# Kernel tuning notes

Measured on AMD Instinct MI355X. Metric: run time of the kernel, lower is better.

## Reference

```python
import jax, jax.numpy as jnp
import numpy as np

B, T = 4, 2048          # batch, seq_len
D, H = 2048, 4096       # input_dim, router hidden_dim
E, O = 16, 2048         # num_experts, expert_output_dim
TAU = 0.5               # forward default tau


def setup_inputs() -> dict:
    key = jax.random.key(0)
    kx, k1, k2, k3, k4, k5, k6 = jax.random.split(key, 7)
    s = 0.02
    return {
        "x": jax.random.normal(kx, (B, T, D), dtype=jnp.float32),
        "W1": jax.random.normal(k1, (D, H), dtype=jnp.float32) * s,
        "b1": jnp.zeros((H,), dtype=jnp.float32),
        "W2": jax.random.normal(k2, (H, E), dtype=jnp.float32) * s,
        "b2": jnp.zeros((E,), dtype=jnp.float32),
        "We": jax.random.normal(k3, (E, D, O), dtype=jnp.float32) * s,
        "be": jnp.zeros((E, O), dtype=jnp.float32),
    }


def reference(x, W1, b1, W2, b2, We, be):
    # Router: Linear -> ReLU -> Linear -> softmax
    h = jax.nn.relu(jnp.einsum("btd,dh->bth", x, W1) + b1)
    logits = jnp.einsum("bth,he->bte", h, W2) + b2
    probs = jax.nn.softmax(logits, axis=-1)                 # [B,T,E]
    max_p = jnp.max(probs, axis=-1, keepdims=True)
    mask = probs >= TAU * max_p                              # [B,T,E] bool
    k_per_token = jnp.sum(mask, axis=-1)                     # [B,T] int
    gates = jnp.where(mask, probs, 0.0)                      # masked router probs
    # Per-expert dense Linear, masked weighted accumulate (E=16 is a fixed,
    # structurally distinct set; loop is over experts, not data dims).
    out = jnp.zeros((B, T, O), dtype=x.dtype)
    for i in range(E):
        expert_out = jnp.einsum("btd,do->bto", x, We[i]) + be[i]
        out = out + gates[..., i:i + 1] * expert_out
    return out, k_per_token
```

## Files before the change

### kernel.cpp

```cpp
#include <hip/hip_runtime.h>
#include <stdint.h>

#define M_TOK 8192
#define DDIM  2048
#define HDIM  4096
#define NEXP  16
#define ODIM  2048

typedef __attribute__((ext_vector_type(8))) __bf16 bf16x8;
typedef __attribute__((ext_vector_type(4))) float  f32x4;

__device__ __forceinline__ unsigned short f2bf(float f) {
    unsigned int u = __float_as_uint(f);
    unsigned int r = (u + 0x7FFFu + ((u >> 16) & 1u)) >> 16;
    return (unsigned short)r;
}
__device__ __forceinline__ float bf2f(unsigned short s) {
    return __uint_as_float(((unsigned int)s) << 16);
}

template <int CTRL>
__device__ __forceinline__ float dpp_mov(float x) {
    return __int_as_float(
        __builtin_amdgcn_update_dpp(0, __float_as_int(x), CTRL, 0xF, 0xF, true));
}
__device__ __forceinline__ float swz_xor4(float x) {
    return __int_as_float(__builtin_amdgcn_ds_swizzle(__float_as_int(x), 0x101F));
}


__global__ void split_x_kernel(const float* __restrict__ x,
                               ushort* __restrict__ xh, ushort* __restrict__ xl) {
    size_t i = ((size_t)blockIdx.x * 256 + threadIdx.x) * 4;
    float4 v = *(const float4*)(x + i);
    float f[4] = {v.x, v.y, v.z, v.w};
    ushort hu[4], lu[4];
#pragma unroll
    for (int u = 0; u < 4; ++u) {
        hu[u] = f2bf(f[u]);
        lu[u] = f2bf(f[u] - bf2f(hu[u]));
    }
    *(ushort4*)(xh + i) = make_ushort4(hu[0], hu[1], hu[2], hu[3]);
    *(ushort4*)(xl + i) = make_ushort4(lu[0], lu[1], lu[2], lu[3]);
}

__global__ void transpose_split_w1_kernel(const float* __restrict__ W1,
                                          ushort* __restrict__ th, ushort* __restrict__ tl) {
    __shared__ float tile[64][65];
    int h0 = (blockIdx.x & 63) * 64;
    int d0 = (blockIdx.x >> 6) * 64;
    int r = threadIdx.x >> 4;
    int c = (threadIdx.x & 15) * 4;
#pragma unroll
    for (int rr = 0; rr < 4; ++rr) {
        int row = rr * 16 + r;
        float4 v = *(const float4*)(W1 + (size_t)(d0 + row) * HDIM + h0 + c);
        tile[row][c + 0] = v.x; tile[row][c + 1] = v.y;
        tile[row][c + 2] = v.z; tile[row][c + 3] = v.w;
    }
    __syncthreads();
#pragma unroll
    for (int rr = 0; rr < 4; ++rr) {
        int hrow = rr * 16 + r;
        ushort hu[4], lu[4];
#pragma unroll
        for (int u = 0; u < 4; ++u) {
            float f = tile[c + u][hrow];
            hu[u] = f2bf(f);
            lu[u] = f2bf(f - bf2f(hu[u]));
        }
        size_t o = (size_t)(h0 + hrow) * DDIM + d0 + c;
        *(ushort4*)(th + o) = make_ushort4(hu[0], hu[1], hu[2], hu[3]);
        *(ushort4*)(tl + o) = make_ushort4(lu[0], lu[1], lu[2], lu[3]);
    }
}

__global__ void transpose_we_kernel(const float* __restrict__ We, ushort* __restrict__ wt) {
    __shared__ float tile[64][65];
    int e = blockIdx.y;
    int o0 = (blockIdx.x & 31) * 64;
    int d0 = (blockIdx.x >> 5) * 64;
    const float* src = We + (size_t)e * DDIM * ODIM;
    ushort* dst = wt + (size_t)e * ODIM * DDIM;
    int r = threadIdx.x >> 4;
    int c = (threadIdx.x & 15) * 4;
#pragma unroll
    for (int rr = 0; rr < 4; ++rr) {
        int row = rr * 16 + r;
        float4 v = *(const float4*)(src + (size_t)(d0 + row) * ODIM + o0 + c);
        tile[row][c + 0] = v.x; tile[row][c + 1] = v.y;
        tile[row][c + 2] = v.z; tile[row][c + 3] = v.w;
    }
    __syncthreads();
#pragma unroll
    for (int rr = 0; rr < 4; ++rr) {
        int orow = rr * 16 + r;
        ushort hu[4];
#pragma unroll
        for (int u = 0; u < 4; ++u) hu[u] = f2bf(tile[c + u][orow]);
        *(ushort4*)(dst + (size_t)(o0 + orow) * DDIM + d0 + c) =
            make_ushort4(hu[0], hu[1], hu[2], hu[3]);
    }
}


__device__ __forceinline__ void stage_tile(const ushort* __restrict__ g0, int ld,
                                           ushort* lds0, int wave, int lane) {
#pragma unroll
    for (int j = 0; j < 4; ++j) {
        int L = wave * 256 + j * 64 + lane;
        int m = L >> 3;
        int kc = (L & 7) ^ (m & 7);
        const ushort* gp = g0 + (size_t)m * ld + kc * 8;
        ushort* lp = lds0 + (size_t)(wave * 256 + j * 64) * 8;
        __builtin_amdgcn_global_load_lds(
            (const __attribute__((address_space(1))) void*)gp,
            (__attribute__((address_space(3))) void*)lp, 16, 0, 0);
    }
}

__device__ __forceinline__ bf16x8 ldfrag(const ushort* lds0, int row, int kc) {
    return *(const bf16x8*)(lds0 + ((row << 3) + (kc ^ (row & 7))) * 8);
}

__device__ __forceinline__ void mfma_step(const ushort* As, const ushort* Bs,
                                          int wm, int wn, int mrow, int q,
                                          f32x4 (&acc)[4][4]) {
#pragma unroll
    for (int s = 0; s < 2; ++s) {
        bf16x8 af[4], bfr[4];
#pragma unroll
        for (int i = 0; i < 4; ++i) af[i] = ldfrag(As, wm + i * 16 + mrow, s * 4 + q);
#pragma unroll
        for (int j = 0; j < 4; ++j) bfr[j] = ldfrag(Bs, wn + j * 16 + mrow, s * 4 + q);
#pragma unroll
        for (int i = 0; i < 4; ++i)
#pragma unroll
            for (int j = 0; j < 4; ++j)
                acc[i][j] = __builtin_amdgcn_mfma_f32_16x16x32_bf16(
                    af[i], bfr[j], acc[i][j], 0, 0, 0);
    }
}

__global__ __launch_bounds__(256, 2) void gemm1_kernel(
    const ushort* __restrict__ xh, const ushort* __restrict__ xl,
    const ushort* __restrict__ wh, const ushort* __restrict__ wl,
    const float* __restrict__ b1, const float* __restrict__ W2,
    float* __restrict__ logits) {
    __shared__ ushort As0[8192];
    __shared__ ushort Bs0[8192];
    __shared__ ushort As1[8192];
    __shared__ ushort Bs1[8192];
    const int tile_m = (blockIdx.x & 63) << 7;
    const int tile_n = (blockIdx.x >> 6) << 7;
    const int tid = threadIdx.x;
    const int wave = tid >> 6, lane = tid & 63;
    const int q = lane >> 4, mrow = lane & 15;
    const int wm = (wave >> 1) << 6, wn = (wave & 1) << 6;
    f32x4 acc[4][4];
#pragma unroll
    for (int i = 0; i < 4; ++i)
#pragma unroll
        for (int j = 0; j < 4; ++j) acc[i][j] = {0.f, 0.f, 0.f, 0.f};

#define SRC_A(t) ((((t) >> 5) == 1 ? xl : xh) + (size_t)tile_m * DDIM + (((t) & 31) << 6))
#define SRC_B(t) ((((t) >> 5) == 2 ? wl : wh) + (size_t)tile_n * DDIM + (((t) & 31) << 6))

    stage_tile(SRC_A(0), DDIM, As0, wave, lane);
    stage_tile(SRC_B(0), DDIM, Bs0, wave, lane);
    __syncthreads();

    for (int it = 0; it < 96; it += 2) {
        stage_tile(SRC_A(it + 1), DDIM, As1, wave, lane);
        stage_tile(SRC_B(it + 1), DDIM, Bs1, wave, lane);
        mfma_step(As0, Bs0, wm, wn, mrow, q, acc);
        __syncthreads();
        if (it + 2 < 96) {
            stage_tile(SRC_A(it + 2), DDIM, As0, wave, lane);
            stage_tile(SRC_B(it + 2), DDIM, Bs0, wave, lane);
        }
        mfma_step(As1, Bs1, wm, wn, mrow, q, acc);
        __syncthreads();
    }
#undef SRC_A
#undef SRC_B

    float b1v[4];
    f32x4 w2r[4][4];
#pragma unroll
    for (int j = 0; j < 4; ++j) {
        const int cc = tile_n + wn + j * 16 + mrow;
        b1v[j] = b1[cc];
        const float4* wp = (const float4*)(W2 + (size_t)cc * NEXP);
#pragma unroll
        for (int qq = 0; qq < 4; ++qq) {
            float4 v = wp[qq];
            w2r[j][qq] = (f32x4){v.x, v.y, v.z, v.w};
        }
    }
    float* part = (float*)As0;
    const int w01 = wave & 1;
    const bool pb0 = (mrow & 1) != 0, pb1 = (mrow & 2) != 0;
    const bool pb2 = (mrow & 4) != 0, pb3 = (mrow & 8) != 0;
    const int E = (mrow & 3) | ((mrow & 8) >> 1) | ((mrow & 4) << 1);
#pragma unroll
    for (int i = 0; i < 4; ++i) {
#pragma unroll
        for (int r = 0; r < 4; ++r) {
            const int rl = wm + i * 16 + q * 4 + r;
            float ll[16];
#pragma unroll
            for (int e = 0; e < 16; ++e) ll[e] = 0.f;
#pragma unroll
            for (int j = 0; j < 4; ++j) {
                float v = acc[i][j][r] + b1v[j];
                v = v > 0.f ? v : 0.f;
#pragma unroll
                for (int e = 0; e < 16; ++e)
                    ll[e] = fmaf(v, w2r[j][e >> 2][e & 3], ll[e]);
            }
            float s1[8];
#pragma unroll
            for (int e2 = 0; e2 < 8; ++e2) {
                float a = ll[2 * e2], b = ll[2 * e2 + 1];
                float y = pb0 ? b : a, z = pb0 ? a : b;
                s1[e2] = y + dpp_mov<0xB1>(z);
            }
            float s2[4];
#pragma unroll
            for (int e2 = 0; e2 < 4; ++e2) {
                float a = s1[2 * e2], b = s1[2 * e2 + 1];
                float y = pb1 ? b : a, z = pb1 ? a : b;
                s2[e2] = y + dpp_mov<0x4E>(z);
            }
            float s3[2];
#pragma unroll
            for (int e2 = 0; e2 < 2; ++e2) {
                float a = s2[2 * e2], b = s2[2 * e2 + 1];
                float y = pb3 ? b : a, z = pb3 ? a : b;
                s3[e2] = y + dpp_mov<0x128>(z);
            }
            {
                float a = s3[0], b = s3[1];
                float y = pb2 ? b : a, z = pb2 ? a : b;
                float fin = y + swz_xor4(z);
                part[(size_t)(w01 * 128 + rl) * 16 + E] = fin;
            }
        }
    }
    __syncthreads();
    for (int idx = tid; idx < 2048; idx += 256) {
        float s = part[idx] + part[2048 + idx];
        atomicAdd(&logits[(size_t)(tile_m + (idx >> 4)) * NEXP + (idx & 15)], s);
    }
}

__global__ void gates_kernel(const float* __restrict__ logits,
                             const float* __restrict__ b2,
                             float* __restrict__ gates, float* __restrict__ kout,
                             int* __restrict__ cnt, int* __restrict__ list) {
    const int t = blockIdx.x * 256 + threadIdx.x;
    float l[16];
    const float4* lp = (const float4*)(logits + (size_t)t * 16);
#pragma unroll
    for (int i = 0; i < 4; ++i) {
        float4 v = lp[i];
        l[i * 4] = v.x; l[i * 4 + 1] = v.y; l[i * 4 + 2] = v.z; l[i * 4 + 3] = v.w;
    }
#pragma unroll
    for (int i = 0; i < 16; ++i) l[i] += b2[i];
    float lmax = l[0];
#pragma unroll
    for (int i = 1; i < 16; ++i) lmax = fmaxf(lmax, l[i]);
    float p[16], S = 0.f;
#pragma unroll
    for (int i = 0; i < 16; ++i) { p[i] = expf(l[i] - lmax); S += p[i]; }
#pragma unroll
    for (int i = 0; i < 16; ++i) p[i] /= S;
    float pmax = p[0];
#pragma unroll
    for (int i = 1; i < 16; ++i) pmax = fmaxf(pmax, p[i]);
    const float thr = 0.5f * pmax;
    int k = 0;
    float g[16];
#pragma unroll
    for (int i = 0; i < 16; ++i) {
        bool m = p[i] >= thr;
        g[i] = m ? p[i] : 0.f;
        k += m ? 1 : 0;
        if (m) {
            int pos = atomicAdd(&cnt[i], 1);
            list[i * M_TOK + pos] = t;
        }
    }
    float4* gp = (float4*)(gates + (size_t)t * 16);
#pragma unroll
    for (int i = 0; i < 4; ++i)
        gp[i] = make_float4(g[i * 4], g[i * 4 + 1], g[i * 4 + 2], g[i * 4 + 3]);
    kout[t] = (float)k;
}

__global__ void init_out_kernel(const float* __restrict__ gates,
                                const float* __restrict__ be, float* __restrict__ out) {
    const int t = blockIdx.x;
    const int tid = threadIdx.x;
    __shared__ float g[16];
    if (tid < 16) g[tid] = gates[(size_t)t * 16 + tid];
    __syncthreads();
    const int c0 = tid * 8;
    float a[8] = {0.f, 0.f, 0.f, 0.f, 0.f, 0.f, 0.f, 0.f};
#pragma unroll
    for (int e = 0; e < 16; ++e) {
        float ge = g[e];
        if (ge != 0.f) {
            float4 v1 = *(const float4*)(be + (size_t)e * ODIM + c0);
            float4 v2 = *(const float4*)(be + (size_t)e * ODIM + c0 + 4);
            a[0] = fmaf(ge, v1.x, a[0]); a[1] = fmaf(ge, v1.y, a[1]);
            a[2] = fmaf(ge, v1.z, a[2]); a[3] = fmaf(ge, v1.w, a[3]);
            a[4] = fmaf(ge, v2.x, a[4]); a[5] = fmaf(ge, v2.y, a[5]);
            a[6] = fmaf(ge, v2.z, a[6]); a[7] = fmaf(ge, v2.w, a[7]);
        }
    }
    *(float4*)(out + (size_t)t * ODIM + c0)     = make_float4(a[0], a[1], a[2], a[3]);
    *(float4*)(out + (size_t)t * ODIM + c0 + 4) = make_float4(a[4], a[5], a[6], a[7]);
}

__global__ __launch_bounds__(256, 3) void moe_sparse_kernel(
    const ushort* __restrict__ xh, const ushort* __restrict__ weT,
    const float* __restrict__ gates, const int* __restrict__ cnt,
    const int* __restrict__ list, float* __restrict__ out) {
    const int bx = blockIdx.x;
    const int e = bx >> 10;
    const int chunk = (bx >> 4) & 63;
    const int ntile = bx & 15;
    const int ce = cnt[e];
    const int row0 = chunk << 7;
    if (row0 >= ce) return;
    const int rows = min(128, ce - row0);

    __shared__ ushort As[8192];
    __shared__ ushort Bs[8192];
    __shared__ int toks[128];
    __shared__ float gv[128];

    const int tid = threadIdx.x;
    if (tid < 128) {
        int t = list[e * M_TOK + row0 + min(tid, rows - 1)];
        toks[tid] = t;
        gv[tid] = gates[(size_t)t * NEXP + e];
    }
    __syncthreads();

    const int wave = tid >> 6, lane = tid & 63;
    const int q = lane >> 4, mrow = lane & 15;
    const int wm = (wave >> 1) << 6, wn = (wave & 1) << 6;

    const ushort* agp[4];
    const ushort* bgp[4];
    ushort* alp[4];
    ushort* blp[4];
    const ushort* wbase = weT + ((size_t)e * ODIM + (ntile << 7)) * DDIM;
#pragma unroll
    for (int j = 0; j < 4; ++j) {
        int L = wave * 256 + j * 64 + lane;
        int m = L >> 3;
        int kc = (L & 7) ^ (m & 7);
        agp[j] = xh + (size_t)toks[m] * DDIM + kc * 8;
        bgp[j] = wbase + (size_t)m * DDIM + kc * 8;
        alp[j] = As + (size_t)L * 8;
        blp[j] = Bs + (size_t)L * 8;
    }

    f32x4 acc[4][4];
#pragma unroll
    for (int i = 0; i < 4; ++i)
#pragma unroll
        for (int j = 0; j < 4; ++j) acc[i][j] = {0.f, 0.f, 0.f, 0.f};

    for (int it = 0; it < 32; ++it) {
        const int k0 = it << 6;
        __syncthreads();
#pragma unroll
        for (int j = 0; j < 4; ++j) {
            __builtin_amdgcn_global_load_lds(
                (const __attribute__((address_space(1))) void*)(agp[j] + k0),
                (__attribute__((address_space(3))) void*)alp[j], 16, 0, 0);
            __builtin_amdgcn_global_load_lds(
                (const __attribute__((address_space(1))) void*)(bgp[j] + k0),
                (__attribute__((address_space(3))) void*)blp[j], 16, 0, 0);
        }
        __syncthreads();
        mfma_step(As, Bs, wm, wn, mrow, q, acc);
    }

#pragma unroll
    for (int i = 0; i < 4; ++i) {
        const int rl = wm + i * 16 + q * 4;
#pragma unroll
        for (int r = 0; r < 4; ++r) {
            const int lrow = rl + r;
            if (lrow < rows) {
                const int t = toks[lrow];
                const float g = gv[lrow];
                float* orow = out + (size_t)t * ODIM + (ntile << 7) + wn + mrow;
#pragma unroll
                for (int j = 0; j < 4; ++j)
                    atomicAdd(orow + j * 16, g * acc[i][j][r]);
            }
        }
    }
}

extern "C" void kernel_launch(void* const* d_in, const int* in_sizes, int n_in,
                              void* d_out, int out_size, void* d_ws, size_t ws_size,
                              hipStream_t stream) {
    const float* x  = (const float*)d_in[0];
    const float* W1 = (const float*)d_in[1];
    const float* b1 = (const float*)d_in[2];
    const float* W2 = (const float*)d_in[3];
    const float* b2 = (const float*)d_in[4];
    const float* We = (const float*)d_in[5];
    const float* be = (const float*)d_in[6];
    float* out  = (float*)d_out;
    float* kout = out + (size_t)M_TOK * ODIM;

    char* ws = (char*)d_ws;
    ushort* x_hi   = (ushort*)(ws);
    ushort* x_lo   = (ushort*)(ws + 33554432);
    ushort* w1t_hi = (ushort*)(ws + 67108864);
    ushort* w1t_lo = (ushort*)(ws + 83886080);
    int*    cnt    = (int*)   (ws + 83886080);
    int*    list   = (int*)   (ws + 83887104);
    ushort* weT    = (ushort*)(ws + 100663296);
    float*  logits = (float*) (ws + 234881024);
    float*  gates  = (float*) (ws + 235405312);

    hipMemsetAsync(logits, 0, (size_t)M_TOK * NEXP * sizeof(float), stream);
    split_x_kernel<<<16384, 256, 0, stream>>>(x, x_hi, x_lo);
    transpose_split_w1_kernel<<<2048, 256, 0, stream>>>(W1, w1t_hi, w1t_lo);
    gemm1_kernel<<<2048, 256, 0, stream>>>(x_hi, x_lo, w1t_hi, w1t_lo, b1, W2, logits);
    hipMemsetAsync(cnt, 0, 64, stream);
    gates_kernel<<<32, 256, 0, stream>>>(logits, b2, gates, kout, cnt, list);
    dim3 gwe(1024, 16);
    transpose_we_kernel<<<gwe, 256, 0, stream>>>(We, weT);
    init_out_kernel<<<M_TOK, 256, 0, stream>>>(gates, be, out);
    moe_sparse_kernel<<<16384, 256, 0, stream>>>(x_hi, weT, gates, cnt, list, out);
}
```

Before: 1.228 ms.

## Enlarge router GEMM tiles to 256x256 with direct global-to-LDS async loads

The router GEMM now uses 256x256 output tiles with 512 threads (8 waves, each 128x64), cutting redundant global reads of x and W1. Tiles are staged with global_load_lds into a swizzled 128KB double buffer, with explicit vmcnt/lgkmcnt waits and barriers so that loading the next K tile overlaps the MFMAs. Partial logits are reduced across four column waves before the atomic adds. The cost is higher register use (acc 8x4) and large LDS use, which limits blocks per CU and could spill.

```diff
diff --git a/kernel.cpp b/kernel.cpp
--- a/kernel.cpp
+++ b/kernel.cpp
@@ -142,54 +142,112 @@
     }
 }
 
-__global__ __launch_bounds__(256, 2) void gemm1_kernel(
+__global__ __launch_bounds__(512, 2) void gemm1_kernel(
     const ushort* __restrict__ xh, const ushort* __restrict__ xl,
     const ushort* __restrict__ wh, const ushort* __restrict__ wl,
     const float* __restrict__ b1, const float* __restrict__ W2,
     float* __restrict__ logits) {
-    __shared__ ushort As0[8192];
-    __shared__ ushort Bs0[8192];
-    __shared__ ushort As1[8192];
-    __shared__ ushort Bs1[8192];
-    const int tile_m = (blockIdx.x & 63) << 7;
-    const int tile_n = (blockIdx.x >> 6) << 7;
+    __shared__ ushort lds[65536];
+    ushort* const A0 = lds;
+    ushort* const B0 = lds + 16384;
+    ushort* const A1 = lds + 32768;
+    ushort* const B1 = lds + 49152;
+
+    const int tile_m = (blockIdx.x >> 4) << 8;
+    const int tile_n = (blockIdx.x & 15) << 8;
     const int tid = threadIdx.x;
     const int wave = tid >> 6, lane = tid & 63;
     const int q = lane >> 4, mrow = lane & 15;
-    const int wm = (wave >> 1) << 6, wn = (wave & 1) << 6;
-    f32x4 acc[4][4];
-#pragma unroll
-    for (int i = 0; i < 4; ++i)
+    const int wr = (wave >> 2) << 7;
+    const int wcb = (wave & 3) << 6;
+
+    unsigned goff[4];
+    int ldso[4];
+#pragma unroll
+    for (int j = 0; j < 4; ++j) {
+        int L = wave * 256 + j * 64 + lane;
+        int m = L >> 3;
+        int kc = (L & 7) ^ (m & 7);
+        goff[j] = (unsigned)m * DDIM + kc * 8;
+        ldso[j] = L * 8;
+    }
+
+    f32x4 acc[8][4];
+#pragma unroll
+    for (int i = 0; i < 8; ++i)
 #pragma unroll
         for (int j = 0; j < 4; ++j) acc[i][j] = {0.f, 0.f, 0.f, 0.f};
 
 #define SRC_A(t) ((((t) >> 5) == 1 ? xl : xh) + (size_t)tile_m * DDIM + (((t) & 31) << 6))
 #define SRC_B(t) ((((t) >> 5) == 2 ? wl : wh) + (size_t)tile_n * DDIM + (((t) & 31) << 6))
-
-    stage_tile(SRC_A(0), DDIM, As0, wave, lane);
-    stage_tile(SRC_B(0), DDIM, Bs0, wave, lane);
-    __syncthreads();
-
-    for (int it = 0; it < 96; it += 2) {
-        stage_tile(SRC_A(it + 1), DDIM, As1, wave, lane);
-        stage_tile(SRC_B(it + 1), DDIM, Bs1, wave, lane);
-        mfma_step(As0, Bs0, wm, wn, mrow, q, acc);
-        __syncthreads();
-        if (it + 2 < 96) {
-            stage_tile(SRC_A(it + 2), DDIM, As0, wave, lane);
-            stage_tile(SRC_B(it + 2), DDIM, Bs0, wave, lane);
-        }
-        mfma_step(As1, Bs1, wm, wn, mrow, q, acc);
-        __syncthreads();
+#define STAGE(srcp, dstp)                                                           \
+    {                                                                               \
+        const ushort* _s = (srcp);                                                  \
+        ushort* _d = (dstp);                                                        \
+        _Pragma("unroll")                                                           \
+        for (int _j = 0; _j < 4; ++_j)                                              \
+            __builtin_amdgcn_global_load_lds(                                       \
+                (const __attribute__((address_space(1))) void*)(_s + goff[_j]),     \
+                (__attribute__((address_space(3))) void*)(_d + ldso[_j]), 16, 0, 0);\
+    }
+
+    STAGE(SRC_A(0), A0); STAGE(SRC_B(0), B0);
+    STAGE(SRC_A(1), A1); STAGE(SRC_B(1), B1);
+    asm volatile("s_waitcnt vmcnt(8)" ::: "memory");
+    __builtin_amdgcn_s_barrier();
+    __builtin_amdgcn_sched_barrier(0);
+
+    for (int kt = 0; kt < 96; ++kt) {
+        ushort* As = (kt & 1) ? A1 : A0;
+        ushort* Bs = (kt & 1) ? B1 : B0;
+        bf16x8 a0[8], a1[8], bv0[4], bv1[4];
+#pragma unroll
+        for (int i = 0; i < 8; ++i) {
+            a0[i] = ldfrag(As, wr + i * 16 + mrow, q);
+            a1[i] = ldfrag(As, wr + i * 16 + mrow, 4 + q);
+        }
+#pragma unroll
+        for (int j = 0; j < 4; ++j) {
+            bv0[j] = ldfrag(Bs, wcb + j * 16 + mrow, q);
+            bv1[j] = ldfrag(Bs, wcb + j * 16 + mrow, 4 + q);
+        }
+        asm volatile("s_waitcnt lgkmcnt(0)" ::: "memory");
+        __builtin_amdgcn_sched_barrier(0);
+        __builtin_amdgcn_s_barrier();
+        __builtin_amdgcn_sched_barrier(0);
+        if (kt + 2 < 96) {
+            STAGE(SRC_A(kt + 2), As);
+            STAGE(SRC_B(kt + 2), Bs);
+        }
+#pragma unroll
+        for (int i = 0; i < 8; ++i)
+#pragma unroll
+            for (int j = 0; j < 4; ++j)
+                acc[i][j] = __builtin_amdgcn_mfma_f32_16x16x32_bf16(
+                    a0[i], bv0[j], acc[i][j], 0, 0, 0);
+#pragma unroll
+        for (int i = 0; i < 8; ++i)
+#pragma unroll
+            for (int j = 0; j < 4; ++j)
+                acc[i][j] = __builtin_amdgcn_mfma_f32_16x16x32_bf16(
+                    a1[i], bv1[j], acc[i][j], 0, 0, 0);
+        if (kt + 2 < 96) {
+            asm volatile("s_waitcnt vmcnt(8)" ::: "memory");
+        } else {
+            asm volatile("s_waitcnt vmcnt(0)" ::: "memory");
+        }
+        __builtin_amdgcn_s_barrier();
+        __builtin_amdgcn_sched_barrier(0);
     }
 #undef SRC_A
 #undef SRC_B
+#undef STAGE
 
     float b1v[4];
     f32x4 w2r[4][4];
 #pragma unroll
     for (int j = 0; j < 4; ++j) {
-        const int cc = tile_n + wn + j * 16 + mrow;
+        const int cc = tile_n + wcb + j * 16 + mrow;
         b1v[j] = b1[cc];
         const float4* wp = (const float4*)(W2 + (size_t)cc * NEXP);
 #pragma unroll
@@ -198,16 +256,17 @@
             w2r[j][qq] = (f32x4){v.x, v.y, v.z, v.w};
         }
     }
-    float* part = (float*)As0;
-    const int w01 = wave & 1;
+    __syncthreads();
+    float* part = (float*)lds;
+    const int pw = wave & 3;
     const bool pb0 = (mrow & 1) != 0, pb1 = (mrow & 2) != 0;
     const bool pb2 = (mrow & 4) != 0, pb3 = (mrow & 8) != 0;
     const int E = (mrow & 3) | ((mrow & 8) >> 1) | ((mrow & 4) << 1);
 #pragma unroll
-    for (int i = 0; i < 4; ++i) {
+    for (int i = 0; i < 8; ++i) {
 #pragma unroll
         for (int r = 0; r < 4; ++r) {
-            const int rl = wm + i * 16 + q * 4 + r;
+            const int rl = wr + i * 16 + q * 4 + r;
             float ll[16];
 #pragma unroll
             for (int e = 0; e < 16; ++e) ll[e] = 0.f;
@@ -244,13 +303,13 @@
                 float a = s3[0], b = s3[1];
                 float y = pb2 ? b : a, z = pb2 ? a : b;
                 float fin = y + swz_xor4(z);
-                part[(size_t)(w01 * 128 + rl) * 16 + E] = fin;
+                part[((size_t)(pw << 8) + rl) * 16 + E] = fin;
             }
         }
     }
     __syncthreads();
-    for (int idx = tid; idx < 2048; idx += 256) {
-        float s = part[idx] + part[2048 + idx];
+    for (int idx = tid; idx < 4096; idx += 512) {
+        float s = part[idx] + part[4096 + idx] + part[8192 + idx] + part[12288 + idx];
         atomicAdd(&logits[(size_t)(tile_m + (idx >> 4)) * NEXP + (idx & 15)], s);
     }
 }
@@ -438,7 +497,7 @@
     hipMemsetAsync(logits, 0, (size_t)M_TOK * NEXP * sizeof(float), stream);
     split_x_kernel<<<16384, 256, 0, stream>>>(x, x_hi, x_lo);
     transpose_split_w1_kernel<<<2048, 256, 0, stream>>>(W1, w1t_hi, w1t_lo);
-    gemm1_kernel<<<2048, 256, 0, stream>>>(x_hi, x_lo, w1t_hi, w1t_lo, b1, W2, logits);
+    gemm1_kernel<<<512, 512, 0, stream>>>(x_hi, x_lo, w1t_hi, w1t_lo, b1, W2, logits);
     hipMemsetAsync(cnt, 0, 64, stream);
     gates_kernel<<<32, 256, 0, stream>>>(logits, b2, gates, kout, cnt, list);
     dim3 gwe(1024, 16);
```

After: 1.198 ms. 2.4% less time.
